# Kernel optimization log

Measured on AMD Instinct MI355X. Metric: run time of the kernel, lower is better.

Reference implementation:

```python
import jax, jax.numpy as jnp
import numpy as np

NEG_SLOPE = 0.2
BN_EPS = 1e-5


def gat_conv(x, W_src, W_dst, att_src, att_dst, bias, src, dst, num_nodes):
    # PyG GATConv, heads=1, concat=True, self-loops already included in (src,dst)
    h_src = x @ W_src                      # [N, H]
    h_dst = x @ W_dst                      # [N, H]
    a_src = h_src @ att_src                # [N]
    a_dst = h_dst @ att_dst                # [N]
    e = jax.nn.leaky_relu(a_src[src] + a_dst[dst], NEG_SLOPE)   # [E]
    # segment softmax over incoming edges of each dst node
    m = jax.ops.segment_max(e, dst, num_segments=num_nodes)     # [N]
    p = jnp.exp(e - m[dst])
    denom = jax.ops.segment_sum(p, dst, num_segments=num_nodes) # [N]
    alpha = p / denom[dst]                                      # [E]
    msgs = alpha[:, None] * h_src[src]                           # [E, H]
    out = jax.ops.segment_sum(msgs, dst, num_segments=num_nodes)
    return out + bias


def setup_inputs() -> dict:
    key = jax.random.key(0)
    ks = jax.random.split(key, 20)
    N, D_IN, H1, H2, FC, C = 100000, 256, 128, 128, 64, 40
    E = 1600000
    inp = {}
    inp['x'] = jax.random.normal(ks[0], (N, D_IN), dtype=jnp.float32)
    inp['edge_index'] = jax.random.randint(ks[1], (2, E), 0, N, dtype=jnp.int64)
    s = 1.0 / np.sqrt(D_IN)
    inp['W1_src'] = jax.random.uniform(ks[2], (D_IN, H1), jnp.float32, -s, s)
    inp['W1_dst'] = jax.random.uniform(ks[3], (D_IN, H1), jnp.float32, -s, s)
    inp['att1_src'] = jax.random.normal(ks[4], (H1,), jnp.float32) * 0.1
    inp['att1_dst'] = jax.random.normal(ks[5], (H1,), jnp.float32) * 0.1
    inp['b1'] = jnp.zeros((H1,), jnp.float32)
    s = 1.0 / np.sqrt(H1)
    inp['W2_src'] = jax.random.uniform(ks[6], (H1, H2), jnp.float32, -s, s)
    inp['W2_dst'] = jax.random.uniform(ks[7], (H1, H2), jnp.float32, -s, s)
    inp['att2_src'] = jax.random.normal(ks[8], (H2,), jnp.float32) * 0.1
    inp['att2_dst'] = jax.random.normal(ks[9], (H2,), jnp.float32) * 0.1
    inp['b2'] = jnp.zeros((H2,), jnp.float32)
    s = 1.0 / np.sqrt(H2)
    inp['fc1_w'] = jax.random.uniform(ks[10], (H2, FC), jnp.float32, -s, s)
    inp['fc1_b'] = jax.random.uniform(ks[11], (FC,), jnp.float32, -s, s)
    inp['gamma'] = jnp.ones((FC,), jnp.float32)
    inp['beta'] = jnp.zeros((FC,), jnp.float32)
    s = 1.0 / np.sqrt(FC)
    inp['fc2_w'] = jax.random.uniform(ks[12], (FC, C), jnp.float32, -s, s)
    inp['fc2_b'] = jax.random.uniform(ks[13], (C,), jnp.float32, -s, s)
    return inp


def reference(x, edge_index, W1_src, W1_dst, att1_src, att1_dst, b1,
              W2_src, W2_dst, att2_src, att2_dst, b2,
              fc1_w, fc1_b, gamma, beta, fc2_w, fc2_b):
    N = x.shape[0]
    loops = jnp.arange(N, dtype=edge_index.dtype)
    src = jnp.concatenate([edge_index[0], loops])
    dst = jnp.concatenate([edge_index[1], loops])
    h = jax.nn.relu(gat_conv(x, W1_src, W1_dst, att1_src, att1_dst, b1, src, dst, N))
    h = jax.nn.relu(gat_conv(h, W2_src, W2_dst, att2_src, att2_dst, b2, src, dst, N))
    h = h @ fc1_w + fc1_b                   # [N, 64]
    mu = jnp.mean(h, axis=0)
    var = jnp.var(h, axis=0)
    h = (h - mu) * jax.lax.rsqrt(var + BN_EPS) * gamma + beta
    h = jax.nn.relu(h)
    h = h @ fc2_w + fc2_b                   # [N, C]
    return jax.nn.log_softmax(h, axis=-1)
```

## Files before the change

### kernel.cpp

```cpp
#include <hip/hip_runtime.h>
#include <cstddef>

#define LSLOPE 0.2f
#define BN_EPS 1e-5f

__device__ __forceinline__ float lrelu(float x) { return x > 0.f ? x : LSLOPE * x; }

using half4 = __attribute__((ext_vector_type(4))) _Float16;
using half8 = __attribute__((ext_vector_type(8))) _Float16;
using f32x4 = __attribute__((ext_vector_type(4))) float;

struct h2 { _Float16 h, l; };
__device__ __forceinline__ h2 split2h(float x) {
  h2 r;
  r.h = (_Float16)x;
  r.l = (_Float16)(x - (float)r.h);
  return r;
}

__device__ __forceinline__ unsigned short f2bf(float x) {
  unsigned u = __float_as_uint(x);
  unsigned r = (u + 0x7fffu + ((u >> 16) & 1u)) >> 16;
  return (unsigned short)r;
}
__device__ __forceinline__ float bflo(unsigned int u) { return __uint_as_float(u << 16); }
__device__ __forceinline__ float bfhi(unsigned int u) { return __uint_as_float(u & 0xffff0000u); }

__global__ void bfrag_k(const float* __restrict__ B, _Float16* __restrict__ bh,
                        _Float16* __restrict__ bl, int K, int M) {
  int t = blockIdx.x * 256 + threadIdx.x;
  int KB = K >> 5;
  int total = (M >> 4) * KB * 64;
  if (t >= total) return;
  int lane = t & 63;
  int ckb  = t >> 6;
  int c  = ckb / KB, kb = ckb % KB;
  int mr = lane & 15, quad = lane >> 4;
  int col = c * 16 + mr;
  size_t obase = (size_t)t * 8;
#pragma unroll
  for (int j = 0; j < 8; ++j) {
    int k = kb * 32 + quad * 8 + j;
    h2 s = split2h(B[(size_t)k * M + col]);
    bh[obase + j] = s.h;
    bl[obase + j] = s.l;
  }
}

template<int MCOLS>
__global__ __launch_bounds__(256) void gemm3h_k(const float* __restrict__ A,
                                                const _Float16* __restrict__ Bh,
                                                const _Float16* __restrict__ Bl,
                                                float* __restrict__ Cf,
                                                unsigned short* __restrict__ Cbf,
                                                const float* __restrict__ attv,
                                                float* __restrict__ asrc,
                                                int N, int K,
                                                const float* __restrict__ bias) {
  constexpr int CT = MCOLS / 16;
  __shared__ __align__(16) _Float16 sAh[2][128 * 32];
  __shared__ __align__(16) _Float16 sAl[2][128 * 32];
  const int tid  = threadIdx.x;
  const int row0 = blockIdx.x * 128;
  const int wv   = tid >> 6;
  const int lane = tid & 63;
  const int quad = lane >> 4;
  const int mr   = lane & 15;
  const int KB   = K >> 5;

  int srow[4], skc[4], soff[4];
  bool sok[4];
#pragma unroll
  for (int cc = 0; cc < 4; ++cc) {
    int s = tid + cc * 256;
    srow[cc] = s >> 3;
    skc[cc]  = (s & 7) << 2;
    soff[cc] = srow[cc] * 32 + ((skc[cc] + srow[cc] * 8) & 31);
    sok[cc]  = (row0 + srow[cc]) < N;
  }

  f32x4 acc[2][CT];
#pragma unroll
  for (int r = 0; r < 2; ++r)
#pragma unroll
    for (int c = 0; c < CT; ++c) acc[r][c] = (f32x4){0.f, 0.f, 0.f, 0.f};

  float4 pf[4];
#pragma unroll
  for (int cc = 0; cc < 4; ++cc)
    pf[cc] = sok[cc] ? *(const float4*)&A[(size_t)(row0 + srow[cc]) * K + skc[cc]]
                     : make_float4(0.f, 0.f, 0.f, 0.f);
#pragma unroll
  for (int cc = 0; cc < 4; ++cc) {
    h2 s0 = split2h(pf[cc].x), s1 = split2h(pf[cc].y), s2 = split2h(pf[cc].z), s3 = split2h(pf[cc].w);
    half4 h4, l4;
    h4[0] = s0.h; h4[1] = s1.h; h4[2] = s2.h; h4[3] = s3.h;
    l4[0] = s0.l; l4[1] = s1.l; l4[2] = s2.l; l4[3] = s3.l;
    *(half4*)&sAh[0][soff[cc]] = h4;
    *(half4*)&sAl[0][soff[cc]] = l4;
  }
  __syncthreads();

  for (int kb = 0; kb < KB; ++kb) {
    const int cur = kb & 1, nxt = cur ^ 1;
    if (kb + 1 < KB) {
      const int kk = (kb + 1) << 5;
#pragma unroll
      for (int cc = 0; cc < 4; ++cc)
        pf[cc] = sok[cc] ? *(const float4*)&A[(size_t)(row0 + srow[cc]) * K + kk + skc[cc]]
                         : make_float4(0.f, 0.f, 0.f, 0.f);
    }

    half8 ah[2], al[2];
#pragma unroll
    for (int r = 0; r < 2; ++r) {
      int row = wv * 32 + r * 16 + mr;
      int off = row * 32 + ((quad + row) & 3) * 8;
      ah[r] = *(const half8*)&sAh[cur][off];
      al[r] = *(const half8*)&sAl[cur][off];
    }
    const _Float16* bb_h = Bh + ((size_t)kb * 64 + lane) * 8;
    const _Float16* bb_l = Bl + ((size_t)kb * 64 + lane) * 8;
    const size_t cstride = (size_t)KB * 512;
#pragma unroll
    for (int c0 = 0; c0 < CT; c0 += 4) {
      half8 bh4[4], bl4[4];
#pragma unroll
      for (int c = 0; c < 4; ++c) {
        size_t o = (size_t)(c0 + c) * cstride;
        bh4[c] = *(const half8*)&bb_h[o];
        bl4[c] = *(const half8*)&bb_l[o];
      }
#pragma unroll
      for (int r = 0; r < 2; ++r)
#pragma unroll
        for (int c = 0; c < 4; ++c) {
          f32x4 a = acc[r][c0 + c];
          a = __builtin_amdgcn_mfma_f32_16x16x32_f16(al[r], bh4[c], a, 0, 0, 0);
          a = __builtin_amdgcn_mfma_f32_16x16x32_f16(ah[r], bl4[c], a, 0, 0, 0);
          a = __builtin_amdgcn_mfma_f32_16x16x32_f16(ah[r], bh4[c], a, 0, 0, 0);
          acc[r][c0 + c] = a;
        }
    }
    if (kb + 1 < KB) {
#pragma unroll
      for (int cc = 0; cc < 4; ++cc) {
        h2 s0 = split2h(pf[cc].x), s1 = split2h(pf[cc].y), s2 = split2h(pf[cc].z), s3 = split2h(pf[cc].w);
        half4 h4, l4;
        h4[0] = s0.h; h4[1] = s1.h; h4[2] = s2.h; h4[3] = s3.h;
        l4[0] = s0.l; l4[1] = s1.l; l4[2] = s2.l; l4[3] = s3.l;
        *(half4*)&sAh[nxt][soff[cc]] = h4;
        *(half4*)&sAl[nxt][soff[cc]] = l4;
      }
    }
    __syncthreads();
  }

  float pa[2][4];
#pragma unroll
  for (int r = 0; r < 2; ++r)
#pragma unroll
    for (int q = 0; q < 4; ++q) pa[r][q] = 0.f;

#pragma unroll
  for (int r = 0; r < 2; ++r)
#pragma unroll
    for (int c = 0; c < CT; ++c) {
      float av = attv ? attv[c * 16 + mr] : 0.f;
#pragma unroll
      for (int q = 0; q < 4; ++q) {
        int grow = row0 + wv * 32 + r * 16 + quad * 4 + q;
        float val = acc[r][c][q];
        if (bias) val += bias[c * 16 + mr];
        if (grow < N) {
          int gcol = c * 16 + mr;
          if (Cf)  Cf[(size_t)grow * MCOLS + gcol] = val;
          if (Cbf) Cbf[(size_t)grow * 128 + gcol] = f2bf(val);
        }
        if (attv) pa[r][q] = fmaf(val, av, pa[r][q]);
      }
    }
  if (attv) {
#pragma unroll
    for (int r = 0; r < 2; ++r)
#pragma unroll
      for (int q = 0; q < 4; ++q) {
        float p2 = pa[r][q];
        p2 += __shfl_xor(p2, 1, 64);
        p2 += __shfl_xor(p2, 2, 64);
        p2 += __shfl_xor(p2, 4, 64);
        p2 += __shfl_xor(p2, 8, 64);
        int grow = row0 + wv * 32 + r * 16 + quad * 4 + q;
        if (mr == 0 && grow < N) asrc[grow] = p2;
      }
  }
}

template<int MCOLS>
__global__ __launch_bounds__(256) void gemm3p_k(const _Float16* __restrict__ Ah,
                                                const _Float16* __restrict__ Al,
                                                const _Float16* __restrict__ Bh,
                                                const _Float16* __restrict__ Bl,
                                                float* __restrict__ Cf,
                                                unsigned short* __restrict__ Cbf,
                                                const float* __restrict__ attv,
                                                float* __restrict__ asrc,
                                                int N, int K,
                                                const float* __restrict__ bias) {
  constexpr int CT = MCOLS / 16;
  __shared__ __align__(16) _Float16 sAh[2][128 * 32];
  __shared__ __align__(16) _Float16 sAl[2][128 * 32];
  const int tid  = threadIdx.x;
  const int row0 = blockIdx.x * 128;
  const int wv   = tid >> 6;
  const int lane = tid & 63;
  const int quad = lane >> 4;
  const int mr   = lane & 15;
  const int KB   = K >> 5;

  int srow[2], sk8[2], soff[2];
  bool sok[2];
#pragma unroll
  for (int cc = 0; cc < 2; ++cc) {
    int s = tid + cc * 256;
    srow[cc] = s >> 2;
    sk8[cc]  = (s & 3) << 3;
    soff[cc] = srow[cc] * 32 + ((sk8[cc] + srow[cc] * 8) & 31);
    sok[cc]  = (row0 + srow[cc]) < N;
  }

  f32x4 acc[2][CT];
#pragma unroll
  for (int r = 0; r < 2; ++r)
#pragma unroll
    for (int c = 0; c < CT; ++c) acc[r][c] = (f32x4){0.f, 0.f, 0.f, 0.f};

  uint4 ph[2], pl[2];
  const uint4 z4 = make_uint4(0u, 0u, 0u, 0u);
#pragma unroll
  for (int cc = 0; cc < 2; ++cc) {
    size_t go = (size_t)(row0 + srow[cc]) * K + sk8[cc];
    ph[cc] = sok[cc] ? *(const uint4*)&Ah[go] : z4;
    pl[cc] = sok[cc] ? *(const uint4*)&Al[go] : z4;
  }
#pragma unroll
  for (int cc = 0; cc < 2; ++cc) {
    *(uint4*)&sAh[0][soff[cc]] = ph[cc];
    *(uint4*)&sAl[0][soff[cc]] = pl[cc];
  }
  __syncthreads();

  for (int kb = 0; kb < KB; ++kb) {
    const int cur = kb & 1, nxt = cur ^ 1;
    if (kb + 1 < KB) {
      const int kk = (kb + 1) << 5;
#pragma unroll
      for (int cc = 0; cc < 2; ++cc) {
        size_t go = (size_t)(row0 + srow[cc]) * K + kk + sk8[cc];
        ph[cc] = sok[cc] ? *(const uint4*)&Ah[go] : z4;
        pl[cc] = sok[cc] ? *(const uint4*)&Al[go] : z4;
      }
    }

    half8 ah[2], al[2];
#pragma unroll
    for (int r = 0; r < 2; ++r) {
      int row = wv * 32 + r * 16 + mr;
      int off = row * 32 + ((quad + row) & 3) * 8;
      ah[r] = *(const half8*)&sAh[cur][off];
      al[r] = *(const half8*)&sAl[cur][off];
    }
    const _Float16* bb_h = Bh + ((size_t)kb * 64 + lane) * 8;
    const _Float16* bb_l = Bl + ((size_t)kb * 64 + lane) * 8;
    const size_t cstride = (size_t)KB * 512;
#pragma unroll
    for (int c0 = 0; c0 < CT; c0 += 4) {
      half8 bh4[4], bl4[4];
#pragma unroll
      for (int c = 0; c < 4; ++c) {
        size_t o = (size_t)(c0 + c) * cstride;
        bh4[c] = *(const half8*)&bb_h[o];
        bl4[c] = *(const half8*)&bb_l[o];
      }
#pragma unroll
      for (int r = 0; r < 2; ++r)
#pragma unroll
        for (int c = 0; c < 4; ++c) {
          f32x4 a = acc[r][c0 + c];
          a = __builtin_amdgcn_mfma_f32_16x16x32_f16(al[r], bh4[c], a, 0, 0, 0);
          a = __builtin_amdgcn_mfma_f32_16x16x32_f16(ah[r], bl4[c], a, 0, 0, 0);
          a = __builtin_amdgcn_mfma_f32_16x16x32_f16(ah[r], bh4[c], a, 0, 0, 0);
          acc[r][c0 + c] = a;
        }
    }
    if (kb + 1 < KB) {
#pragma unroll
      for (int cc = 0; cc < 2; ++cc) {
        *(uint4*)&sAh[nxt][soff[cc]] = ph[cc];
        *(uint4*)&sAl[nxt][soff[cc]] = pl[cc];
      }
    }
    __syncthreads();
  }

  float pa[2][4];
#pragma unroll
  for (int r = 0; r < 2; ++r)
#pragma unroll
    for (int q = 0; q < 4; ++q) pa[r][q] = 0.f;

#pragma unroll
  for (int r = 0; r < 2; ++r)
#pragma unroll
    for (int c = 0; c < CT; ++c) {
      float av = attv ? attv[c * 16 + mr] : 0.f;
#pragma unroll
      for (int q = 0; q < 4; ++q) {
        int grow = row0 + wv * 32 + r * 16 + quad * 4 + q;
        float val = acc[r][c][q];
        if (bias) val += bias[c * 16 + mr];
        if (grow < N) {
          int gcol = c * 16 + mr;
          if (Cf)  Cf[(size_t)grow * MCOLS + gcol] = val;
          if (Cbf) Cbf[(size_t)grow * 128 + gcol] = f2bf(val);
        }
        if (attv) pa[r][q] = fmaf(val, av, pa[r][q]);
      }
    }
  if (attv) {
#pragma unroll
    for (int r = 0; r < 2; ++r)
#pragma unroll
      for (int q = 0; q < 4; ++q) {
        float p2 = pa[r][q];
        p2 += __shfl_xor(p2, 1, 64);
        p2 += __shfl_xor(p2, 2, 64);
        p2 += __shfl_xor(p2, 4, 64);
        p2 += __shfl_xor(p2, 8, 64);
        int grow = row0 + wv * 32 + r * 16 + quad * 4 + q;
        if (mr == 0 && grow < N) asrc[grow] = p2;
      }
  }
}

__global__ __launch_bounds__(256) void matvec_k(const float* __restrict__ A, const float* __restrict__ v,
                                                float* __restrict__ out, int R, int K) {
  int w = (blockIdx.x * blockDim.x + threadIdx.x) >> 6;
  int lane = threadIdx.x & 63;
  if (w >= R) return;
  const float* row = A + (size_t)w * K;
  float s = 0.f;
  for (int k = lane; k < K; k += 64) s = fmaf(row[k], v[k], s);
#pragma unroll
  for (int off = 32; off; off >>= 1) s += __shfl_xor(s, off, 64);
  if (lane == 0) out[w] = s;
}

__global__ void deg_count_k(const int* __restrict__ edst, int E, int N, int* __restrict__ deg) {
  int i = blockIdx.x * 256 + threadIdx.x;
  if (i >= E + N) return;
  int d = (i < E) ? edst[i] : (i - E);
  atomicAdd(&deg[d], 1);
}

__global__ __launch_bounds__(1024) void scan1_k(const int* __restrict__ deg, int n,
                                                int* __restrict__ ex, int* __restrict__ bsum) {
  __shared__ int sm[1024];
  int t = threadIdx.x;
  int idx = blockIdx.x * 1024 + t;
  int v = (idx < n) ? deg[idx] : 0;
  sm[t] = v;
  __syncthreads();
  for (int off = 1; off < 1024; off <<= 1) {
    int tv = (t >= off) ? sm[t - off] : 0;
    __syncthreads();
    sm[t] += tv;
    __syncthreads();
  }
  if (idx < n) ex[idx] = sm[t] - v;
  if (t == 1023) bsum[blockIdx.x] = sm[t];
}

__global__ void scan2_k(int* __restrict__ bsum, int nb) {
  if (threadIdx.x == 0 && blockIdx.x == 0) {
    int run = 0;
    for (int b = 0; b < nb; ++b) { int x = bsum[b]; bsum[b] = run; run += x; }
  }
}

__global__ void scan3_k(int* __restrict__ ex, const int* __restrict__ bsum, int n, int total,
                        int* __restrict__ cursor) {
  int idx = blockIdx.x * 256 + threadIdx.x;
  if (idx < n) {
    int v = ex[idx] + bsum[idx >> 10];
    ex[idx] = v;
    cursor[idx] = v;
  }
  if (idx == 0) ex[n] = total;
}

__global__ void scatter_range_k(const int* __restrict__ esrc, const int* __restrict__ edst,
                                int E, int N, int d0, int d1,
                                int* __restrict__ cursor, int* __restrict__ csr_src) {
  int i = blockIdx.x * 256 + threadIdx.x;
  if (i >= E + N) return;
  int d = (i < E) ? edst[i] : (i - E);
  if (d < d0 || d >= d1) return;
  int s = (i < E) ? esrc[i] : d;
  int pos = atomicAdd(&cursor[d], 1);
  csr_src[pos] = s;
}

__global__ __launch_bounds__(256) void gat_agg_k(const unsigned short* __restrict__ hbf,
                                                 const float* __restrict__ a_src,
                                                 const float* __restrict__ a_dst, const int* __restrict__ rowstart,
                                                 const int* __restrict__ csr_src, const float* __restrict__ bias,
                                                 _Float16* __restrict__ oh, _Float16* __restrict__ ol,
                                                 const float* __restrict__ wvd, float* __restrict__ ad_out,
                                                 int N) {
  int w = (blockIdx.x * blockDim.x + threadIdx.x) >> 6;
  int lane = threadIdx.x & 63;
  if (w >= N) return;
  int s0 = rowstart[w];
  int s1 = rowstart[w + 1];
  int deg = s1 - s0;
  float ad = a_dst[w];

  int sA = 0;
  float eA = -3.0e38f;
  if (lane < deg) {
    sA = csr_src[s0 + lane];
    eA = lrelu(a_src[sA] + ad);
  }
  float m = eA;
  for (int j = s0 + 64 + lane; j < s1; j += 64) {
    int s = csr_src[j];
    m = fmaxf(m, lrelu(a_src[s] + ad));
  }
#pragma unroll
  for (int off = 32; off; off >>= 1) m = fmaxf(m, __shfl_xor(m, off, 64));

  float preg = (lane < deg) ? __expf(eA - m) : 0.f;
  float den = preg;
  for (int j = s0 + 64 + lane; j < s1; j += 64) {
    int s = csr_src[j];
    den += __expf(lrelu(a_src[s] + ad) - m);
  }
#pragma unroll
  for (int off = 32; off; off >>= 1) den += __shfl_xor(den, off, 64);
  float inv = 1.f / den;

  const int q  = lane >> 4;
  const int sl = lane & 15;
  const uint4* hrow4 = (const uint4*)hbf;
  float acc[8];
#pragma unroll
  for (int i = 0; i < 8; ++i) acc[i] = 0.f;

  int lim  = deg < 64 ? deg : 64;
  int lim4 = (lim + 3) & ~3;
  for (int jj = 0; jj < lim4; jj += 4) {
    int e = jj + q;
    int s = __shfl(sA, e, 64);
    float wgt = __shfl(preg, e, 64) * inv;
    uint4 u = hrow4[(size_t)s * 16 + sl];
    acc[0] = fmaf(wgt, bflo(u.x), acc[0]);
    acc[1] = fmaf(wgt, bfhi(u.x), acc[1]);
    acc[2] = fmaf(wgt, bflo(u.y), acc[2]);
    acc[3] = fmaf(wgt, bfhi(u.y), acc[3]);
    acc[4] = fmaf(wgt, bflo(u.z), acc[4]);
    acc[5] = fmaf(wgt, bfhi(u.z), acc[5]);
    acc[6] = fmaf(wgt, bflo(u.w), acc[6]);
    acc[7] = fmaf(wgt, bfhi(u.w), acc[7]);
  }
  for (int j = s0 + 64 + q; j < s1; j += 4) {
    int s = csr_src[j];
    float wgt = __expf(lrelu(a_src[s] + ad) - m) * inv;
    uint4 u = hrow4[(size_t)s * 16 + sl];
    acc[0] = fmaf(wgt, bflo(u.x), acc[0]);
    acc[1] = fmaf(wgt, bfhi(u.x), acc[1]);
    acc[2] = fmaf(wgt, bflo(u.y), acc[2]);
    acc[3] = fmaf(wgt, bfhi(u.y), acc[3]);
    acc[4] = fmaf(wgt, bflo(u.z), acc[4]);
    acc[5] = fmaf(wgt, bfhi(u.z), acc[5]);
    acc[6] = fmaf(wgt, bflo(u.w), acc[6]);
    acc[7] = fmaf(wgt, bfhi(u.w), acc[7]);
  }
#pragma unroll
  for (int i = 0; i < 8; ++i) {
    acc[i] += __shfl_xor(acc[i], 16, 64);
    acc[i] += __shfl_xor(acc[i], 32, 64);
  }
  if (q == 0) {
    float4 b0 = *(const float4*)&bias[8 * sl];
    float4 b1 = *(const float4*)&bias[8 * sl + 4];
    float v[8];
    v[0] = fmaxf(acc[0] + b0.x, 0.f);
    v[1] = fmaxf(acc[1] + b0.y, 0.f);
    v[2] = fmaxf(acc[2] + b0.z, 0.f);
    v[3] = fmaxf(acc[3] + b0.w, 0.f);
    v[4] = fmaxf(acc[4] + b1.x, 0.f);
    v[5] = fmaxf(acc[5] + b1.y, 0.f);
    v[6] = fmaxf(acc[6] + b1.z, 0.f);
    v[7] = fmaxf(acc[7] + b1.w, 0.f);
    half8 vh, vl;
#pragma unroll
    for (int i = 0; i < 8; ++i) {
      h2 s = split2h(v[i]);
      vh[i] = s.h;
      vl[i] = s.l;
    }
    size_t base = (size_t)w * 128 + 8 * sl;
    *(half8*)&oh[base] = vh;
    *(half8*)&ol[base] = vl;
    if (wvd) {
      float4 w0 = *(const float4*)&wvd[8 * sl];
      float4 w1 = *(const float4*)&wvd[8 * sl + 4];
      float dd = v[0] * w0.x + v[1] * w0.y + v[2] * w0.z + v[3] * w0.w
               + v[4] * w1.x + v[5] * w1.y + v[6] * w1.z + v[7] * w1.w;
      dd += __shfl_xor(dd, 1, 64);
      dd += __shfl_xor(dd, 2, 64);
      dd += __shfl_xor(dd, 4, 64);
      dd += __shfl_xor(dd, 8, 64);
      if (sl == 0) ad_out[w] = dd;
    }
  }
}

__global__ __launch_bounds__(256) void bn_stats_k(const float* __restrict__ z, int N,
                                                  float* __restrict__ sums, float* __restrict__ sumsq) {
  __shared__ float ls[256], lq[256];
  int col = threadIdx.x & 63;
  int rg = threadIdx.x >> 6;
  float s = 0.f, q = 0.f;
  for (int r = blockIdx.x * 4 + rg; r < N; r += gridDim.x * 4) {
    float v = z[(size_t)r * 64 + col];
    s += v;
    q = fmaf(v, v, q);
  }
  ls[threadIdx.x] = s;
  lq[threadIdx.x] = q;
  __syncthreads();
  if (threadIdx.x < 64) {
    s = ls[col] + ls[col + 64] + ls[col + 128] + ls[col + 192];
    q = lq[col] + lq[col + 64] + lq[col + 128] + lq[col + 192];
    atomicAdd(&sums[col], s);
    atomicAdd(&sumsq[col], q);
  }
}

__global__ void bn_finalize_k(const float* __restrict__ sums, const float* __restrict__ sumsq,
                              const float* __restrict__ gamma, const float* __restrict__ beta,
                              int N, float* __restrict__ scale, float* __restrict__ shift) {
  int c = threadIdx.x;
  if (c >= 64) return;
  float mean = sums[c] / (float)N;
  float var = sumsq[c] / (float)N - mean * mean;
  float rs = rsqrtf(var + BN_EPS);
  float sc = gamma[c] * rs;
  scale[c] = sc;
  shift[c] = beta[c] - mean * sc;
}

__global__ __launch_bounds__(256) void fc2_lsm_k(const float* __restrict__ z, const float* __restrict__ scale,
                                                 const float* __restrict__ shift, const float* __restrict__ w,
                                                 const float* __restrict__ b, float* __restrict__ out, int N) {
  int n = blockIdx.x * 256 + threadIdx.x;
  if (n >= N) return;
  float o[40];
#pragma unroll
  for (int c = 0; c < 40; ++c) o[c] = b[c];
  const float* zr = z + (size_t)n * 64;
  for (int k = 0; k < 64; ++k) {
    float v = fmaxf(fmaf(zr[k], scale[k], shift[k]), 0.f);
#pragma unroll
    for (int c = 0; c < 40; ++c) o[c] = fmaf(v, w[k * 40 + c], o[c]);
  }
  float mx = o[0];
#pragma unroll
  for (int c = 1; c < 40; ++c) mx = fmaxf(mx, o[c]);
  float s = 0.f;
#pragma unroll
  for (int c = 0; c < 40; ++c) s += __expf(o[c] - mx);
  float ls = __logf(s);
  float* orow = out + (size_t)n * 40;
#pragma unroll
  for (int c = 0; c < 40; ++c) orow[c] = o[c] - mx - ls;
}

static inline char* al16(char* p) { return (char*)(((size_t)p + 15) & ~(size_t)15); }

extern "C" void kernel_launch(void* const* d_in, const int* in_sizes, int n_in,
                              void* d_out, int out_size, void* d_ws, size_t ws_size,
                              hipStream_t stream) {
  const float* x     = (const float*)d_in[0];
  const int*   eidx  = (const int*)d_in[1];
  const float* W1s   = (const float*)d_in[2];
  const float* W1d   = (const float*)d_in[3];
  const float* att1s = (const float*)d_in[4];
  const float* att1d = (const float*)d_in[5];
  const float* b1    = (const float*)d_in[6];
  const float* W2s   = (const float*)d_in[7];
  const float* W2d   = (const float*)d_in[8];
  const float* att2s = (const float*)d_in[9];
  const float* att2d = (const float*)d_in[10];
  const float* b2    = (const float*)d_in[11];
  const float* fc1w  = (const float*)d_in[12];
  const float* fc1b  = (const float*)d_in[13];
  const float* gamma = (const float*)d_in[14];
  const float* beta  = (const float*)d_in[15];
  const float* fc2w  = (const float*)d_in[16];
  const float* fc2b  = (const float*)d_in[17];
  float* out = (float*)d_out;

  const int N  = in_sizes[0] / 256;
  const int E  = in_sizes[1] / 2;
  const int ET = E + N;
  const int DIN = 256, H1 = 128;

  char* p = (char*)d_ws;
  unsigned short* bhA = (unsigned short*)p; p += (size_t)N * 128 * 2;
  _Float16* hAh = (_Float16*)p;  p += (size_t)N * 128 * 2;
  _Float16* hAl = (_Float16*)p;  p += (size_t)N * 128 * 2;
  float* hF = (float*)p;         p += (size_t)N * 64 * 4;
  int* deg      = (int*)p;     p += (size_t)N * 4;
  int* rowstart = (int*)p;     p += (size_t)(N + 1) * 4;
  int* cursor   = (int*)p;     p += (size_t)N * 4;
  int* csr_src  = (int*)p;     p += (size_t)ET * 4;
  float* a_src  = (float*)p;   p += (size_t)N * 4;
  float* a_dst  = (float*)p;   p += (size_t)N * 4;
  float* a_dst2 = (float*)p;   p += (size_t)N * 4;
  float* wvd1   = (float*)p;   p += 256 * 4;
  float* wvd2   = (float*)p;   p += 128 * 4;
  float* sums   = (float*)p;   p += 64 * 4;
  float* sumsq  = (float*)p;   p += 64 * 4;
  float* scale  = (float*)p;   p += 64 * 4;
  float* shift  = (float*)p;   p += 64 * 4;
  int* bsum     = (int*)p;     p += 256 * 4;
  p = al16(p);
  _Float16* B1h = (_Float16*)p; p += (size_t)256 * 128 * 2;
  _Float16* B1l = (_Float16*)p; p += (size_t)256 * 128 * 2;
  _Float16* B2h = (_Float16*)p; p += (size_t)128 * 128 * 2;
  _Float16* B2l = (_Float16*)p; p += (size_t)128 * 128 * 2;
  _Float16* Bfh = (_Float16*)p; p += (size_t)128 * 64 * 2;
  _Float16* Bfl = (_Float16*)p; p += (size_t)128 * 64 * 2;

  const int* esrc = eidx;
  const int* edst = eidx + E;

  hipMemsetAsync(deg, 0, (size_t)N * 4, stream);
  deg_count_k<<<(ET + 255) / 256, 256, 0, stream>>>(edst, E, N, deg);
  int nb = (N + 1023) / 1024;
  scan1_k<<<nb, 1024, 0, stream>>>(deg, N, rowstart, bsum);
  scan2_k<<<1, 64, 0, stream>>>(bsum, nb);
  scan3_k<<<(N + 255) / 256, 256, 0, stream>>>(rowstart, bsum, N, ET, cursor);
  {
    const int NR = 8;
    int step = (N + NR - 1) / NR;
    for (int r = 0; r < NR; ++r) {
      int d0 = r * step;
      int d1 = d0 + step < N ? d0 + step : N;
      scatter_range_k<<<(ET + 255) / 256, 256, 0, stream>>>(esrc, edst, E, N, d0, d1, cursor, csr_src);
    }
  }

  bfrag_k<<<16, 256, 0, stream>>>(W1s, B1h, B1l, 256, 128);
  bfrag_k<<<8, 256, 0, stream>>>(W2s, B2h, B2l, 128, 128);
  bfrag_k<<<4, 256, 0, stream>>>(fc1w, Bfh, Bfl, 128, 64);
  matvec_k<<<64, 256, 0, stream>>>(W1d, att1d, wvd1, 256, 128);
  matvec_k<<<32, 256, 0, stream>>>(W2d, att2d, wvd2, 128, 128);

  const int gemm_blocks = (N + 127) / 128;

  gemm3h_k<128><<<gemm_blocks, 256, 0, stream>>>(x, B1h, B1l, (float*)nullptr, bhA, att1s, a_src,
                                                 N, DIN, (const float*)nullptr);
  matvec_k<<<(N + 3) / 4, 256, 0, stream>>>(x, wvd1, a_dst, N, DIN);
  gat_agg_k<<<(N + 3) / 4, 256, 0, stream>>>(bhA, a_src, a_dst, rowstart, csr_src, b1,
                                             hAh, hAl, wvd2, a_dst2, N);

  gemm3p_k<128><<<gemm_blocks, 256, 0, stream>>>(hAh, hAl, B2h, B2l, (float*)nullptr, bhA, att2s, a_src,
                                                 N, H1, (const float*)nullptr);
  gat_agg_k<<<(N + 3) / 4, 256, 0, stream>>>(bhA, a_src, a_dst2, rowstart, csr_src, b2,
                                             hAh, hAl, (const float*)nullptr, (float*)nullptr, N);

  gemm3p_k<64><<<gemm_blocks, 256, 0, stream>>>(hAh, hAl, Bfh, Bfl, hF, (unsigned short*)nullptr,
                                                (const float*)nullptr, (float*)nullptr, N, H1, fc1b);
  hipMemsetAsync(sums, 0, 128 * sizeof(float), stream);
  bn_stats_k<<<512, 256, 0, stream>>>(hF, N, sums, sumsq);
  bn_finalize_k<<<1, 64, 0, stream>>>(sums, sumsq, gamma, beta, N, scale, shift);
  fc2_lsm_k<<<(N + 255) / 256, 256, 0, stream>>>(hF, scale, shift, fc2w, fc2b, out, N);
}
```

Baseline: 763.9 us.

## Fuse prep kernels, fold dst-attention matvec into GEMM, drop tiny launches

Merges the weight-fragment and matvec prep kernels into a single launch. Computes the layer-1 destination attention dot product inside the first GEMM from the already-split A tiles, removing a separate pass over x. Folds scan2 into scan3 by having each block sum the block totals itself, folds the BN finalize into the fc2 kernel, and merges the two memsets by moving sums next to deg. This removes several launches and one full read of x, at the cost of extra FMAs in the GEMM and redundant prefix sums per block.

```diff
diff --git a/kernel.cpp b/kernel.cpp
--- a/kernel.cpp
+++ b/kernel.cpp
@@ -26,12 +26,9 @@
 __device__ __forceinline__ float bflo(unsigned int u) { return __uint_as_float(u << 16); }
 __device__ __forceinline__ float bfhi(unsigned int u) { return __uint_as_float(u & 0xffff0000u); }
 
-__global__ void bfrag_k(const float* __restrict__ B, _Float16* __restrict__ bh,
-                        _Float16* __restrict__ bl, int K, int M) {
-  int t = blockIdx.x * 256 + threadIdx.x;
+__device__ __forceinline__ void bfrag_body(const float* __restrict__ B, _Float16* __restrict__ bh,
+                                           _Float16* __restrict__ bl, int K, int M, int t) {
   int KB = K >> 5;
-  int total = (M >> 4) * KB * 64;
-  if (t >= total) return;
   int lane = t & 63;
   int ckb  = t >> 6;
   int c  = ckb / KB, kb = ckb % KB;
@@ -45,6 +42,35 @@
     bh[obase + j] = s.h;
     bl[obase + j] = s.l;
   }
+}
+
+__device__ __forceinline__ void matvec_body(const float* __restrict__ A, const float* __restrict__ v,
+                                            float* __restrict__ out, int R, int K, int t) {
+  int w = t >> 6;
+  int lane = t & 63;
+  if (w >= R) return;
+  const float* row = A + (size_t)w * K;
+  float s = 0.f;
+  for (int k = lane; k < K; k += 64) s = fmaf(row[k], v[k], s);
+#pragma unroll
+  for (int off = 32; off; off >>= 1) s += __shfl_xor(s, off, 64);
+  if (lane == 0) out[w] = s;
+}
+
+__global__ __launch_bounds__(256) void prep_k(const float* __restrict__ W1s, const float* __restrict__ W2s,
+                                              const float* __restrict__ fc1w,
+                                              const float* __restrict__ W1d, const float* __restrict__ att1d,
+                                              const float* __restrict__ W2d, const float* __restrict__ att2d,
+                                              _Float16* B1h, _Float16* B1l, _Float16* B2h, _Float16* B2l,
+                                              _Float16* Bfh, _Float16* Bfl,
+                                              float* wvd1, float* wvd2) {
+  int b = blockIdx.x;
+  int tid = threadIdx.x;
+  if (b < 16)       bfrag_body(W1s, B1h, B1l, 256, 128, b * 256 + tid);
+  else if (b < 24)  bfrag_body(W2s, B2h, B2l, 128, 128, (b - 16) * 256 + tid);
+  else if (b < 28)  bfrag_body(fc1w, Bfh, Bfl, 128, 64, (b - 24) * 256 + tid);
+  else if (b < 92)  matvec_body(W1d, att1d, wvd1, 256, 128, (b - 28) * 256 + tid);
+  else              matvec_body(W2d, att2d, wvd2, 128, 128, (b - 92) * 256 + tid);
 }
 
 template<int MCOLS>
@@ -55,6 +81,8 @@
                                                 unsigned short* __restrict__ Cbf,
                                                 const float* __restrict__ attv,
                                                 float* __restrict__ asrc,
+                                                const float* __restrict__ wvd,
+                                                float* __restrict__ adout,
                                                 int N, int K,
                                                 const float* __restrict__ bias) {
   constexpr int CT = MCOLS / 16;
@@ -84,6 +112,7 @@
   for (int r = 0; r < 2; ++r)
 #pragma unroll
     for (int c = 0; c < CT; ++c) acc[r][c] = (f32x4){0.f, 0.f, 0.f, 0.f};
+  float pad[2] = {0.f, 0.f};
 
   float4 pf[4];
 #pragma unroll
@@ -103,11 +132,12 @@
 
   for (int kb = 0; kb < KB; ++kb) {
     const int cur = kb & 1, nxt = cur ^ 1;
+    const int kk = kb << 5;
     if (kb + 1 < KB) {
-      const int kk = (kb + 1) << 5;
+      const int kn = (kb + 1) << 5;
 #pragma unroll
       for (int cc = 0; cc < 4; ++cc)
-        pf[cc] = sok[cc] ? *(const float4*)&A[(size_t)(row0 + srow[cc]) * K + kk + skc[cc]]
+        pf[cc] = sok[cc] ? *(const float4*)&A[(size_t)(row0 + srow[cc]) * K + kn + skc[cc]]
                          : make_float4(0.f, 0.f, 0.f, 0.f);
     }
 
@@ -118,6 +148,20 @@
       int off = row * 32 + ((quad + row) & 3) * 8;
       ah[r] = *(const half8*)&sAh[cur][off];
       al[r] = *(const half8*)&sAl[cur][off];
+    }
+    if (wvd) {
+      const float* wp = wvd + kk + quad * 8;
+#pragma unroll
+      for (int r = 0; r < 2; ++r) {
+        float d = 0.f;
+#pragma unroll
+        for (int j = 0; j < 8; ++j) {
+          float av = wp[j];
+          d = fmaf((float)ah[r][j], av, d);
+          d = fmaf((float)al[r][j], av, d);
+        }
+        pad[r] += d;
+      }
     }
     const _Float16* bb_h = Bh + ((size_t)kb * 64 + lane) * 8;
     const _Float16* bb_l = Bl + ((size_t)kb * 64 + lane) * 8;
@@ -193,6 +237,16 @@
         int grow = row0 + wv * 32 + r * 16 + quad * 4 + q;
         if (mr == 0 && grow < N) asrc[grow] = p2;
       }
+  }
+  if (wvd) {
+#pragma unroll
+    for (int r = 0; r < 2; ++r) {
+      float d = pad[r];
+      d += __shfl_xor(d, 16, 64);
+      d += __shfl_xor(d, 32, 64);
+      int grow = row0 + wv * 32 + r * 16 + mr;
+      if (quad == 0 && grow < N) adout[grow] = d;
+    }
   }
 }
 
@@ -343,19 +397,6 @@
   }
 }
 
-__global__ __launch_bounds__(256) void matvec_k(const float* __restrict__ A, const float* __restrict__ v,
-                                                float* __restrict__ out, int R, int K) {
-  int w = (blockIdx.x * blockDim.x + threadIdx.x) >> 6;
-  int lane = threadIdx.x & 63;
-  if (w >= R) return;
-  const float* row = A + (size_t)w * K;
-  float s = 0.f;
-  for (int k = lane; k < K; k += 64) s = fmaf(row[k], v[k], s);
-#pragma unroll
-  for (int off = 32; off; off >>= 1) s += __shfl_xor(s, off, 64);
-  if (lane == 0) out[w] = s;
-}
-
 __global__ void deg_count_k(const int* __restrict__ edst, int E, int N, int* __restrict__ deg) {
   int i = blockIdx.x * 256 + threadIdx.x;
   if (i >= E + N) return;
@@ -381,18 +422,20 @@
   if (t == 1023) bsum[blockIdx.x] = sm[t];
 }
 
-__global__ void scan2_k(int* __restrict__ bsum, int nb) {
-  if (threadIdx.x == 0 && blockIdx.x == 0) {
-    int run = 0;
-    for (int b = 0; b < nb; ++b) { int x = bsum[b]; bsum[b] = run; run += x; }
-  }
-}
-
-__global__ void scan3_k(int* __restrict__ ex, const int* __restrict__ bsum, int n, int total,
+__global__ void scan3_k(int* __restrict__ ex, const int* __restrict__ bsum, int n, int nb, int total,
                         int* __restrict__ cursor) {
+  __shared__ int pbase[2];
   int idx = blockIdx.x * 256 + threadIdx.x;
+  int bin0 = (blockIdx.x * 256) >> 10;
+  if (threadIdx.x < 2) {
+    int b = bin0 + threadIdx.x;
+    int s = 0;
+    for (int i = 0; i < b && i < nb; ++i) s += bsum[i];
+    pbase[threadIdx.x] = s;
+  }
+  __syncthreads();
   if (idx < n) {
-    int v = ex[idx] + bsum[idx >> 10];
+    int v = ex[idx] + pbase[(idx >> 10) - bin0];
     ex[idx] = v;
     cursor[idx] = v;
   }
@@ -549,22 +592,23 @@
   }
 }
 
-__global__ void bn_finalize_k(const float* __restrict__ sums, const float* __restrict__ sumsq,
-                              const float* __restrict__ gamma, const float* __restrict__ beta,
-                              int N, float* __restrict__ scale, float* __restrict__ shift) {
-  int c = threadIdx.x;
-  if (c >= 64) return;
-  float mean = sums[c] / (float)N;
-  float var = sumsq[c] / (float)N - mean * mean;
-  float rs = rsqrtf(var + BN_EPS);
-  float sc = gamma[c] * rs;
-  scale[c] = sc;
-  shift[c] = beta[c] - mean * sc;
-}
-
-__global__ __launch_bounds__(256) void fc2_lsm_k(const float* __restrict__ z, const float* __restrict__ scale,
-                                                 const float* __restrict__ shift, const float* __restrict__ w,
-                                                 const float* __restrict__ b, float* __restrict__ out, int N) {
+__global__ __launch_bounds__(256) void fc2_lsm_k(const float* __restrict__ z,
+                                                 const float* __restrict__ sums, const float* __restrict__ sumsq,
+                                                 const float* __restrict__ gamma, const float* __restrict__ beta,
+                                                 const float* __restrict__ w,
+                                                 const float* __restrict__ b, float* __restrict__ out,
+                                                 int N, float invN) {
+  __shared__ float ssc[64], ssh[64];
+  if (threadIdx.x < 64) {
+    int c = threadIdx.x;
+    float mean = sums[c] * invN;
+    float var = sumsq[c] * invN - mean * mean;
+    float rs = rsqrtf(var + BN_EPS);
+    float sc = gamma[c] * rs;
+    ssc[c] = sc;
+    ssh[c] = beta[c] - mean * sc;
+  }
+  __syncthreads();
   int n = blockIdx.x * 256 + threadIdx.x;
   if (n >= N) return;
   float o[40];
@@ -572,7 +616,7 @@
   for (int c = 0; c < 40; ++c) o[c] = b[c];
   const float* zr = z + (size_t)n * 64;
   for (int k = 0; k < 64; ++k) {
-    float v = fmaxf(fmaf(zr[k], scale[k], shift[k]), 0.f);
+    float v = fmaxf(fmaf(zr[k], ssc[k], ssh[k]), 0.f);
 #pragma unroll
     for (int c = 0; c < 40; ++c) o[c] = fmaf(v, w[k * 40 + c], o[c]);
   }
@@ -619,11 +663,13 @@
   const int DIN = 256, H1 = 128;
 
   char* p = (char*)d_ws;
+  int* deg      = (int*)p;     p += (size_t)N * 4;
+  float* sums   = (float*)p;   p += 64 * 4;
+  float* sumsq  = (float*)p;   p += 64 * 4;
   unsigned short* bhA = (unsigned short*)p; p += (size_t)N * 128 * 2;
   _Float16* hAh = (_Float16*)p;  p += (size_t)N * 128 * 2;
   _Float16* hAl = (_Float16*)p;  p += (size_t)N * 128 * 2;
   float* hF = (float*)p;         p += (size_t)N * 64 * 4;
-  int* deg      = (int*)p;     p += (size_t)N * 4;
   int* rowstart = (int*)p;     p += (size_t)(N + 1) * 4;
   int* cursor   = (int*)p;     p += (size_t)N * 4;
   int* csr_src  = (int*)p;     p += (size_t)ET * 4;
@@ -632,10 +678,6 @@
   float* a_dst2 = (float*)p;   p += (size_t)N * 4;
   float* wvd1   = (float*)p;   p += 256 * 4;
   float* wvd2   = (float*)p;   p += 128 * 4;
-  float* sums   = (float*)p;   p += 64 * 4;
-  float* sumsq  = (float*)p;   p += 64 * 4;
-  float* scale  = (float*)p;   p += 64 * 4;
-  float* shift  = (float*)p;   p += 64 * 4;
   int* bsum     = (int*)p;     p += 256 * 4;
   p = al16(p);
   _Float16* B1h = (_Float16*)p; p += (size_t)256 * 128 * 2;
@@ -648,12 +690,12 @@
   const int* esrc = eidx;
   const int* edst = eidx + E;
 
-  hipMemsetAsync(deg, 0, (size_t)N * 4, stream);
+  hipMemsetAsync(deg, 0, (size_t)N * 4 + 512, stream);
+
   deg_count_k<<<(ET + 255) / 256, 256, 0, stream>>>(edst, E, N, deg);
   int nb = (N + 1023) / 1024;
   scan1_k<<<nb, 1024, 0, stream>>>(deg, N, rowstart, bsum);
-  scan2_k<<<1, 64, 0, stream>>>(bsum, nb);
-  scan3_k<<<(N + 255) / 256, 256, 0, stream>>>(rowstart, bsum, N, ET, cursor);
+  scan3_k<<<(N + 255) / 256, 256, 0, stream>>>(rowstart, bsum, N, nb, ET, cursor);
   {
     const int NR = 8;
     int step = (N + NR - 1) / NR;
@@ -664,17 +706,13 @@
     }
   }
 
-  bfrag_k<<<16, 256, 0, stream>>>(W1s, B1h, B1l, 256, 128);
-  bfrag_k<<<8, 256, 0, stream>>>(W2s, B2h, B2l, 128, 128);
-  bfrag_k<<<4, 256, 0, stream>>>(fc1w, Bfh, Bfl, 128, 64);
-  matvec_k<<<64, 256, 0, stream>>>(W1d, att1d, wvd1, 256, 128);
-  matvec_k<<<32, 256, 0, stream>>>(W2d, att2d, wvd2, 128, 128);
+  prep_k<<<124, 256, 0, stream>>>(W1s, W2s, fc1w, W1d, att1d, W2d, att2d,
+                                  B1h, B1l, B2h, B2l, Bfh, Bfl, wvd1, wvd2);
 
   const int gemm_blocks = (N + 127) / 128;
 
   gemm3h_k<128><<<gemm_blocks, 256, 0, stream>>>(x, B1h, B1l, (float*)nullptr, bhA, att1s, a_src,
-                                                 N, DIN, (const float*)nullptr);
-  matvec_k<<<(N + 3) / 4, 256, 0, stream>>>(x, wvd1, a_dst, N, DIN);
+                                                 wvd1, a_dst, N, DIN, (const float*)nullptr);
   gat_agg_k<<<(N + 3) / 4, 256, 0, stream>>>(bhA, a_src, a_dst, rowstart, csr_src, b1,
                                              hAh, hAl, wvd2, a_dst2, N);
 
@@ -685,8 +723,7 @@
 
   gemm3p_k<64><<<gemm_blocks, 256, 0, stream>>>(hAh, hAl, Bfh, Bfl, hF, (unsigned short*)nullptr,
                                                 (const float*)nullptr, (float*)nullptr, N, H1, fc1b);
-  hipMemsetAsync(sums, 0, 128 * sizeof(float), stream);
   bn_stats_k<<<512, 256, 0, stream>>>(hF, N, sums, sumsq);
-  bn_finalize_k<<<1, 64, 0, stream>>>(sums, sumsq, gamma, beta, N, scale, shift);
-  fc2_lsm_k<<<(N + 255) / 256, 256, 0, stream>>>(hF, scale, shift, fc2w, fc2b, out, N);
-}
+  fc2_lsm_k<<<(N + 255) / 256, 256, 0, stream>>>(hF, sums, sumsq, gamma, beta, fc2w, fc2b, out,
+                                                 N, 1.0f / (float)N);
+}
```

Result: faster. 717.1 us (-6.1%).
